# Kernel tuning notes

Hardware: AMD Instinct MI355X
Metric: run time of the kernel (lower is better)

## Reference

```python
import jax, jax.numpy as jnp
import numpy as np

N = 50000    # nodes
E = 640000   # edges (avg degree ~12.8)
D = 128      # feature dim (input = hidden = output)
L = 3        # num_layers
BN_EPS = 1e-5


def setup_inputs() -> dict:
    key = jax.random.key(0)
    ks = jax.random.split(key, 6)
    x = jax.random.normal(ks[0], (N, D), dtype=jnp.float32)
    edge_index = jax.random.randint(ks[1], (2, E), 0, N, dtype=jnp.int32)
    s = 1.0 / np.sqrt(D)
    # Weights stored as (in, out); equivalent to torch Linear's x @ W.T with W:(out,in).
    W1 = jax.random.normal(ks[2], (L, D, D), dtype=jnp.float32) * s
    b1 = jnp.zeros((L, D), dtype=jnp.float32)
    gamma = jnp.ones((L, D), dtype=jnp.float32)   # BatchNorm weight
    beta = jnp.zeros((L, D), dtype=jnp.float32)   # BatchNorm bias
    W2 = jax.random.normal(ks[3], (L, D, D), dtype=jnp.float32) * s
    b2 = jnp.zeros((L, D), dtype=jnp.float32)
    return {"x": x, "W1": W1, "b1": b1, "gamma": gamma, "beta": beta,
            "W2": W2, "b2": b2, "edge_index": edge_index}


def reference(x, W1, b1, gamma, beta, W2, b2, edge_index):
    src = edge_index[0]
    dst = edge_index[1]
    h = x
    for i in range(L):
        # GINConv aggregation: sum of source-node features into destinations, eps=0
        agg = jax.ops.segment_sum(h[src], dst, num_segments=N)   # [N, D]
        z = h + agg                                              # (1+eps)*x + sum_j x_j
        # MLP: Linear -> BatchNorm1d (training stats) -> ReLU -> Linear
        z = z @ W1[i] + b1[i]
        mu = jnp.mean(z, axis=0)
        var = jnp.mean((z - mu) ** 2, axis=0)                    # biased var (torch BN)
        z = (z - mu) * jax.lax.rsqrt(var + BN_EPS) * gamma[i] + beta[i]
        z = jax.nn.relu(z)
        z = z @ W2[i] + b2[i]
        # inter-layer ReLU (dropout_rate=0 -> identity)
        h = jax.nn.relu(z) if i < L - 1 else z
    return h
```

## Files before the change

kernel.cpp:

```cpp
#include <hip/hip_runtime.h>

#define D 128
#define BN_EPS 1e-5f
#define ELLW 64

typedef __bf16 bf16_t;
typedef __bf16 bf16x8 __attribute__((ext_vector_type(8)));
typedef __bf16 bf16x4 __attribute__((ext_vector_type(4)));
typedef __bf16 bf16x2 __attribute__((ext_vector_type(2)));
typedef float floatx4 __attribute__((ext_vector_type(4)));

__global__ void prep(const float* __restrict__ x, bf16_t* __restrict__ hb,
                     const float* __restrict__ W1, const float* __restrict__ W2,
                     bf16_t* __restrict__ Wsw, int* __restrict__ deg,
                     float* __restrict__ stats, int N, int n4) {
  int i = blockIdx.x * blockDim.x + threadIdx.x;
  if (i < n4) {
    float4 v = ((const float4*)x)[i];
    bf16x4 p;
    p[0] = (bf16_t)v.x; p[1] = (bf16_t)v.y; p[2] = (bf16_t)v.z; p[3] = (bf16_t)v.w;
    *(bf16x4*)(hb + (size_t)4 * i) = p;
  }
  if (i < N) deg[i] = 0;
  if (i < 768) stats[i] = 0.f;
  if (i < 6 * 16384) {
    int mat = i >> 14;
    int kn = i & 16383;
    int k = kn >> 7;
    int n = kn & 127;
    const float* Wm = (mat < 3) ? (W1 + (size_t)mat * 16384)
                                : (W2 + (size_t)(mat - 3) * 16384);
    float v = Wm[kn];
    int f = ((n >> 4) << 2) | (k >> 5);
    int ln = (((k >> 3) & 3) << 4) | (n & 15);
    int j = k & 7;
    Wsw[(size_t)mat * 16384 + ((f << 6) + ln) * 8 + j] = (bf16_t)v;
  }
}

__global__ void ell_fill(const int* __restrict__ src, const int* __restrict__ dst,
                         int* __restrict__ deg, int* __restrict__ ell, int E) {
  int e = blockIdx.x * blockDim.x + threadIdx.x;
  if (e < E) {
    int d = dst[e];
    int slot = atomicAdd(&deg[d], 1);
    if (slot < ELLW) ell[(size_t)d * ELLW + slot] = src[e];
  }
}

__global__ __launch_bounds__(256) void aggregate(
    const bf16_t* __restrict__ h, bf16_t* __restrict__ z,
    const int* __restrict__ ell, const int* __restrict__ deg, int Nn) {
  int node = blockIdx.x * 4 + (threadIdx.x >> 6);
  if (node >= Nn) return;
  int lane = threadIdx.x & 63;
  int off = lane << 1;
  int dg = deg[node]; if (dg > ELLW) dg = ELLW;
  const int* nb = ell + (size_t)node * ELLW;

  bf16x2 sv = *(const bf16x2*)(h + (size_t)node * D + off);
  float a0x = (float)sv[0], a0y = (float)sv[1];
  float a1x = 0.f, a1y = 0.f, a2x = 0.f, a2y = 0.f, a3x = 0.f, a3y = 0.f;
  int e = 0;
  for (; e + 4 <= dg; e += 4) {
    int4 i4 = *(const int4*)(nb + e);
    bf16x2 v0 = *(const bf16x2*)(h + (size_t)i4.x * D + off);
    bf16x2 v1 = *(const bf16x2*)(h + (size_t)i4.y * D + off);
    bf16x2 v2 = *(const bf16x2*)(h + (size_t)i4.z * D + off);
    bf16x2 v3 = *(const bf16x2*)(h + (size_t)i4.w * D + off);
    a0x += (float)v0[0]; a0y += (float)v0[1];
    a1x += (float)v1[0]; a1y += (float)v1[1];
    a2x += (float)v2[0]; a2y += (float)v2[1];
    a3x += (float)v3[0]; a3y += (float)v3[1];
  }
  for (; e < dg; ++e) {
    bf16x2 v = *(const bf16x2*)(h + (size_t)nb[e] * D + off);
    a0x += (float)v[0]; a0y += (float)v[1];
  }
  a0x += a1x + a2x + a3x;
  a0y += a1y + a2y + a3y;
  bf16x2 o;
  o[0] = (bf16_t)a0x; o[1] = (bf16_t)a0y;
  *(bf16x2*)(z + (size_t)node * D + off) = o;
}

__global__ __launch_bounds__(256) void gemm1_stats(
    const bf16_t* __restrict__ Z, const bf16_t* __restrict__ Wsw,
    const float* __restrict__ bias, bf16_t* __restrict__ Yf,
    float* __restrict__ stats, int nStrips, int N) {
  __shared__ bf16_t T[64][136];
  __shared__ float sred[256];
  const int t = threadIdx.x;
  const int wv = t >> 6;
  const int lane = t & 63;
  const int l15 = lane & 15;
  const int quad = lane >> 4;
  const int strip = blockIdx.x * 4 + wv;
  const bool active = strip < nStrips;

  sred[t] = 0.f;

  bf16x8 a[4];
  const int row = strip * 16 + l15;
  if (active && row < N) {
#pragma unroll
    for (int kc = 0; kc < 4; ++kc)
      a[kc] = *(const bf16x8*)(Z + (size_t)row * D + kc * 32 + quad * 8);
  } else {
#pragma unroll
    for (int kc = 0; kc < 4; ++kc)
#pragma unroll
      for (int j = 0; j < 8; ++j) a[kc][j] = (bf16_t)0.f;
  }

  floatx4 acc[8];
#pragma unroll
  for (int nt = 0; nt < 8; ++nt) {
    float bv = bias[nt * 16 + l15];
    acc[nt] = (floatx4){bv, bv, bv, bv};
  }

#pragma unroll
  for (int nt = 0; nt < 8; ++nt) {
#pragma unroll
    for (int kc = 0; kc < 4; ++kc) {
      bf16x8 b = *(const bf16x8*)(Wsw + (size_t)((nt * 4 + kc) * 64 + lane) * 8);
      acc[nt] = __builtin_amdgcn_mfma_f32_16x16x32_bf16(a[kc], b, acc[nt], 0, 0, 0);
    }
  }

  const int lr = wv * 16 + quad * 4;
#pragma unroll
  for (int nt = 0; nt < 8; ++nt) {
    int c = nt * 16 + l15;
#pragma unroll
    for (int r = 0; r < 4; ++r) T[lr + r][c] = (bf16_t)acc[nt][r];
  }
  __syncthreads();
  if (active) {
#pragma unroll
    for (int kc = 0; kc < 4; ++kc) {
      bf16x8 yv = *(const bf16x8*)&T[wv * 16 + l15][kc * 32 + quad * 8];
      *(bf16x8*)(Yf + ((size_t)(strip * 4 + kc) * 64 + lane) * 8) = yv;
    }
  }

  const int rowBase = strip * 16 + quad * 4;
#pragma unroll
  for (int nt = 0; nt < 8; ++nt) {
    int c = nt * 16 + l15;
    float s = 0.f, q = 0.f;
    if (active) {
#pragma unroll
      for (int r = 0; r < 4; ++r) {
        if (rowBase + r < N) {
          float v = acc[nt][r];
          s += v; q += v * v;
        }
      }
    }
    s += __shfl_xor(s, 16); s += __shfl_xor(s, 32);
    q += __shfl_xor(q, 16); q += __shfl_xor(q, 32);
    if (quad == 0) {
      atomicAdd(&sred[c], s);
      atomicAdd(&sred[128 + c], q);
    }
  }
  __syncthreads();
  atomicAdd(&stats[t], sred[t]);
}

__global__ __launch_bounds__(256) void mlp2(
    const bf16_t* __restrict__ Yf, const float* __restrict__ stats,
    const float* __restrict__ gamma, const float* __restrict__ beta,
    const bf16_t* __restrict__ Wsw, const float* __restrict__ bias,
    void* __restrict__ outp, int nStrips, int N, float invN,
    int relu_out, int fp32_out) {
  __shared__ float abL[256];
  const int t = threadIdx.x;
  if (t < 128) {
    float mu = stats[t] * invN;
    float var = fmaxf(stats[128 + t] * invN - mu * mu, 0.f);
    float a = gamma[t] * rsqrtf(var + BN_EPS);
    abL[t] = a;
    abL[128 + t] = beta[t] - mu * a;
  }
  __syncthreads();

  const int wv = t >> 6;
  const int lane = t & 63;
  const int l15 = lane & 15;
  const int quad = lane >> 4;
  const int strip = blockIdx.x * 4 + wv;
  if (strip >= nStrips) return;

  bf16x8 a2[4];
#pragma unroll
  for (int kc = 0; kc < 4; ++kc) {
    bf16x8 y = *(const bf16x8*)(Yf + ((size_t)(strip * 4 + kc) * 64 + lane) * 8);
#pragma unroll
    for (int j = 0; j < 8; ++j) {
      int c = kc * 32 + quad * 8 + j;
      float v = fmaxf(fmaf((float)y[j], abL[c], abL[128 + c]), 0.f);
      a2[kc][j] = (bf16_t)v;
    }
  }

  floatx4 acc[8];
#pragma unroll
  for (int nt = 0; nt < 8; ++nt) {
    float bv = bias[nt * 16 + l15];
    acc[nt] = (floatx4){bv, bv, bv, bv};
  }

#pragma unroll
  for (int nt = 0; nt < 8; ++nt) {
#pragma unroll
    for (int kc = 0; kc < 4; ++kc) {
      bf16x8 b = *(const bf16x8*)(Wsw + (size_t)((nt * 4 + kc) * 64 + lane) * 8);
      acc[nt] = __builtin_amdgcn_mfma_f32_16x16x32_bf16(a2[kc], b, acc[nt], 0, 0, 0);
    }
  }

  const int rowBase = strip * 16 + quad * 4;
  if (fp32_out) {
    float* out = (float*)outp;
#pragma unroll
    for (int nt = 0; nt < 8; ++nt) {
      int c = nt * 16 + l15;
#pragma unroll
      for (int r = 0; r < 4; ++r) {
        int row = rowBase + r;
        if (row < N) {
          float v = acc[nt][r];
          if (relu_out) v = fmaxf(v, 0.f);
          out[(size_t)row * D + c] = v;
        }
      }
    }
  } else {
    bf16_t* out = (bf16_t*)outp;
#pragma unroll
    for (int nt = 0; nt < 8; ++nt) {
      int c = nt * 16 + l15;
#pragma unroll
      for (int r = 0; r < 4; ++r) {
        int row = rowBase + r;
        if (row < N) {
          float v = acc[nt][r];
          if (relu_out) v = fmaxf(v, 0.f);
          out[(size_t)row * D + c] = (bf16_t)v;
        }
      }
    }
  }
}

extern "C" void kernel_launch(void* const* d_in, const int* in_sizes, int n_in,
                              void* d_out, int out_size, void* d_ws, size_t ws_size,
                              hipStream_t stream) {
  const float* x     = (const float*)d_in[0];
  const float* W1    = (const float*)d_in[1];
  const float* b1    = (const float*)d_in[2];
  const float* gamma = (const float*)d_in[3];
  const float* beta  = (const float*)d_in[4];
  const float* W2    = (const float*)d_in[5];
  const float* b2    = (const float*)d_in[6];
  const int*   ei    = (const int*)d_in[7];

  const int N = in_sizes[0] / D;
  const int E = in_sizes[7] / 2;
  const int* src = ei;
  const int* dst = ei + E;
  float* out = (float*)d_out;

  char* ws = (char*)d_ws;
  size_t bufBytes = (size_t)N * D * sizeof(bf16_t);
  bf16_t* hb   = (bf16_t*)ws;
  bf16_t* zb   = (bf16_t*)(ws + bufBytes);
  bf16_t* Yf   = (bf16_t*)(ws + 2 * bufBytes);
  int*    ell  = (int*)(ws + 3 * bufBytes);
  int*    deg  = (int*)((char*)ell + (size_t)N * ELLW * sizeof(int));
  float*  stats = (float*)((char*)deg + (size_t)N * sizeof(int));
  bf16_t* Wsw  = (bf16_t*)((char*)stats + 768 * sizeof(float));

  const int n4 = N * D / 4;
  const int prepBlocks = (n4 + 255) / 256;
  const int eb = (E + 255) / 256;
  const int aggBlocks = (N + 3) / 4;
  const int nStrips = (N + 15) / 16;
  const int gemmBlocks = (nStrips + 3) / 4;
  const float invN = 1.f / (float)N;

  prep<<<prepBlocks, 256, 0, stream>>>(x, hb, W1, W2, Wsw, deg, stats, N, n4);
  ell_fill<<<eb, 256, 0, stream>>>(src, dst, deg, ell, E);

  for (int i = 0; i < 3; ++i) {
    float* st = stats + (size_t)i * 256;
    aggregate<<<aggBlocks, 256, 0, stream>>>(hb, zb, ell, deg, N);
    gemm1_stats<<<gemmBlocks, 256, 0, stream>>>(
        zb, Wsw + (size_t)i * 16384, b1 + (size_t)i * D, Yf, st, nStrips, N);
    void* Ob = (i == 2) ? d_out : (void*)hb;
    mlp2<<<gemmBlocks, 256, 0, stream>>>(
        Yf, st, gamma + (size_t)i * D, beta + (size_t)i * D,
        Wsw + (size_t)(i + 3) * 16384, b2 + (size_t)i * D,
        Ob, nStrips, N, invN, (i < 2) ? 1 : 0, (i == 2) ? 1 : 0);
  }
}
```

Measured before the change: 342.9 us.

## Fuse both MLP GEMMs into one kernel with grid-wide barrier for BN stats

Merges gemm1_stats and mlp2 into a single kernel that keeps the first GEMM output in shared memory. An atomic-counter spin barrier waits for global BatchNorm statistics before applying normalization and the second GEMM. This removes the intermediate Yf buffer write/read and one kernel launch per layer. It relies on all 782 blocks being co-resident, otherwise it can deadlock, and it adds spin-wait cost.

```diff
diff --git a/kernel.cpp b/kernel.cpp
--- a/kernel.cpp
+++ b/kernel.cpp
@@ -13,7 +13,8 @@
 __global__ void prep(const float* __restrict__ x, bf16_t* __restrict__ hb,
                      const float* __restrict__ W1, const float* __restrict__ W2,
                      bf16_t* __restrict__ Wsw, int* __restrict__ deg,
-                     float* __restrict__ stats, int N, int n4) {
+                     float* __restrict__ stats, int* __restrict__ cnts,
+                     int N, int n4) {
   int i = blockIdx.x * blockDim.x + threadIdx.x;
   if (i < n4) {
     float4 v = ((const float4*)x)[i];
@@ -23,6 +24,7 @@
   }
   if (i < N) deg[i] = 0;
   if (i < 768) stats[i] = 0.f;
+  if (i < 3) cnts[i] = 0;
   if (i < 6 * 16384) {
     int mat = i >> 14;
     int kn = i & 16383;
@@ -84,12 +86,17 @@
   *(bf16x2*)(z + (size_t)node * D + off) = o;
 }
 
-__global__ __launch_bounds__(256) void gemm1_stats(
-    const bf16_t* __restrict__ Z, const bf16_t* __restrict__ Wsw,
-    const float* __restrict__ bias, bf16_t* __restrict__ Yf,
-    float* __restrict__ stats, int nStrips, int N) {
+__global__ __launch_bounds__(256) void fused_mlp(
+    const bf16_t* __restrict__ zb, const bf16_t* __restrict__ Ws1,
+    const bf16_t* __restrict__ Ws2, const float* __restrict__ b1l,
+    const float* __restrict__ b2l, const float* __restrict__ gl,
+    const float* __restrict__ btl, float* __restrict__ st,
+    int* __restrict__ ctr, void* __restrict__ outp,
+    int nStrips, int N, float invN, int relu_out, int fp32_out, int nBlocks) {
   __shared__ bf16_t T[64][136];
   __shared__ float sred[256];
+  __shared__ float abL[256];
+
   const int t = threadIdx.x;
   const int wv = t >> 6;
   const int lane = t & 63;
@@ -105,7 +112,7 @@
   if (active && row < N) {
 #pragma unroll
     for (int kc = 0; kc < 4; ++kc)
-      a[kc] = *(const bf16x8*)(Z + (size_t)row * D + kc * 32 + quad * 8);
+      a[kc] = *(const bf16x8*)(zb + (size_t)row * D + kc * 32 + quad * 8);
   } else {
 #pragma unroll
     for (int kc = 0; kc < 4; ++kc)
@@ -116,15 +123,14 @@
   floatx4 acc[8];
 #pragma unroll
   for (int nt = 0; nt < 8; ++nt) {
-    float bv = bias[nt * 16 + l15];
+    float bv = b1l[nt * 16 + l15];
     acc[nt] = (floatx4){bv, bv, bv, bv};
   }
-
 #pragma unroll
   for (int nt = 0; nt < 8; ++nt) {
 #pragma unroll
     for (int kc = 0; kc < 4; ++kc) {
-      bf16x8 b = *(const bf16x8*)(Wsw + (size_t)((nt * 4 + kc) * 64 + lane) * 8);
+      bf16x8 b = *(const bf16x8*)(Ws1 + (size_t)((nt * 4 + kc) * 64 + lane) * 8);
       acc[nt] = __builtin_amdgcn_mfma_f32_16x16x32_bf16(a[kc], b, acc[nt], 0, 0, 0);
     }
   }
@@ -136,16 +142,9 @@
 #pragma unroll
     for (int r = 0; r < 4; ++r) T[lr + r][c] = (bf16_t)acc[nt][r];
   }
-  __syncthreads();
-  if (active) {
-#pragma unroll
-    for (int kc = 0; kc < 4; ++kc) {
-      bf16x8 yv = *(const bf16x8*)&T[wv * 16 + l15][kc * 32 + quad * 8];
-      *(bf16x8*)(Yf + ((size_t)(strip * 4 + kc) * 64 + lane) * 8) = yv;
-    }
-  }
 
   const int rowBase = strip * 16 + quad * 4;
+  __syncthreads();
 #pragma unroll
   for (int nt = 0; nt < 8; ++nt) {
     int c = nt * 16 + l15;
@@ -167,89 +166,83 @@
     }
   }
   __syncthreads();
-  atomicAdd(&stats[t], sred[t]);
-}
-
-__global__ __launch_bounds__(256) void mlp2(
-    const bf16_t* __restrict__ Yf, const float* __restrict__ stats,
-    const float* __restrict__ gamma, const float* __restrict__ beta,
-    const bf16_t* __restrict__ Wsw, const float* __restrict__ bias,
-    void* __restrict__ outp, int nStrips, int N, float invN,
-    int relu_out, int fp32_out) {
-  __shared__ float abL[256];
-  const int t = threadIdx.x;
+  atomicAdd(&st[t], sred[t]);
+  __threadfence();
+  __syncthreads();
+  if (t == 0) {
+    __hip_atomic_fetch_add(ctr, 1, __ATOMIC_RELEASE, __HIP_MEMORY_SCOPE_AGENT);
+    while (__hip_atomic_load(ctr, __ATOMIC_ACQUIRE, __HIP_MEMORY_SCOPE_AGENT)
+           < nBlocks) { }
+  }
+  __syncthreads();
+
   if (t < 128) {
-    float mu = stats[t] * invN;
-    float var = fmaxf(stats[128 + t] * invN - mu * mu, 0.f);
-    float a = gamma[t] * rsqrtf(var + BN_EPS);
-    abL[t] = a;
-    abL[128 + t] = beta[t] - mu * a;
-  }
-  __syncthreads();
-
-  const int wv = t >> 6;
-  const int lane = t & 63;
-  const int l15 = lane & 15;
-  const int quad = lane >> 4;
-  const int strip = blockIdx.x * 4 + wv;
-  if (strip >= nStrips) return;
-
-  bf16x8 a2[4];
-#pragma unroll
-  for (int kc = 0; kc < 4; ++kc) {
-    bf16x8 y = *(const bf16x8*)(Yf + ((size_t)(strip * 4 + kc) * 64 + lane) * 8);
-#pragma unroll
-    for (int j = 0; j < 8; ++j) {
-      int c = kc * 32 + quad * 8 + j;
-      float v = fmaxf(fmaf((float)y[j], abL[c], abL[128 + c]), 0.f);
-      a2[kc][j] = (bf16_t)v;
-    }
-  }
-
-  floatx4 acc[8];
-#pragma unroll
-  for (int nt = 0; nt < 8; ++nt) {
-    float bv = bias[nt * 16 + l15];
-    acc[nt] = (floatx4){bv, bv, bv, bv};
-  }
-
-#pragma unroll
-  for (int nt = 0; nt < 8; ++nt) {
+    float s = __hip_atomic_load(&st[t], __ATOMIC_RELAXED, __HIP_MEMORY_SCOPE_AGENT);
+    float q = __hip_atomic_load(&st[128 + t], __ATOMIC_RELAXED, __HIP_MEMORY_SCOPE_AGENT);
+    float mu = s * invN;
+    float var = fmaxf(q * invN - mu * mu, 0.f);
+    float av = gl[t] * rsqrtf(var + BN_EPS);
+    abL[t] = av;
+    abL[128 + t] = btl[t] - mu * av;
+  }
+  __syncthreads();
+
+  if (active) {
+    bf16x8 a2[4];
 #pragma unroll
     for (int kc = 0; kc < 4; ++kc) {
-      bf16x8 b = *(const bf16x8*)(Wsw + (size_t)((nt * 4 + kc) * 64 + lane) * 8);
-      acc[nt] = __builtin_amdgcn_mfma_f32_16x16x32_bf16(a2[kc], b, acc[nt], 0, 0, 0);
-    }
-  }
-
-  const int rowBase = strip * 16 + quad * 4;
-  if (fp32_out) {
-    float* out = (float*)outp;
+      bf16x8 y = *(const bf16x8*)&T[wv * 16 + l15][kc * 32 + quad * 8];
+#pragma unroll
+      for (int j = 0; j < 8; ++j) {
+        int c = kc * 32 + quad * 8 + j;
+        float v = fmaxf(fmaf((float)y[j], abL[c], abL[128 + c]), 0.f);
+        a2[kc][j] = (bf16_t)v;
+      }
+    }
+
+    floatx4 acc2[8];
 #pragma unroll
     for (int nt = 0; nt < 8; ++nt) {
-      int c = nt * 16 + l15;
-#pragma unroll
-      for (int r = 0; r < 4; ++r) {
-        int row = rowBase + r;
-        if (row < N) {
-          float v = acc[nt][r];
-          if (relu_out) v = fmaxf(v, 0.f);
-          out[(size_t)row * D + c] = v;
+      float bv = b2l[nt * 16 + l15];
+      acc2[nt] = (floatx4){bv, bv, bv, bv};
+    }
+#pragma unroll
+    for (int nt = 0; nt < 8; ++nt) {
+#pragma unroll
+      for (int kc = 0; kc < 4; ++kc) {
+        bf16x8 b = *(const bf16x8*)(Ws2 + (size_t)((nt * 4 + kc) * 64 + lane) * 8);
+        acc2[nt] = __builtin_amdgcn_mfma_f32_16x16x32_bf16(a2[kc], b, acc2[nt], 0, 0, 0);
+      }
+    }
+
+    if (fp32_out) {
+      float* out = (float*)outp;
+#pragma unroll
+      for (int nt = 0; nt < 8; ++nt) {
+        int c = nt * 16 + l15;
+#pragma unroll
+        for (int r = 0; r < 4; ++r) {
+          int rw = rowBase + r;
+          if (rw < N) {
+            float v = acc2[nt][r];
+            if (relu_out) v = fmaxf(v, 0.f);
+            out[(size_t)rw * D + c] = v;
+          }
         }
       }
-    }
-  } else {
-    bf16_t* out = (bf16_t*)outp;
-#pragma unroll
-    for (int nt = 0; nt < 8; ++nt) {
-      int c = nt * 16 + l15;
-#pragma unroll
-      for (int r = 0; r < 4; ++r) {
-        int row = rowBase + r;
-        if (row < N) {
-          float v = acc[nt][r];
-          if (relu_out) v = fmaxf(v, 0.f);
-          out[(size_t)row * D + c] = (bf16_t)v;
+    } else {
+      bf16_t* out = (bf16_t*)outp;
+#pragma unroll
+      for (int nt = 0; nt < 8; ++nt) {
+        int c = nt * 16 + l15;
+#pragma unroll
+        for (int r = 0; r < 4; ++r) {
+          int rw = rowBase + r;
+          if (rw < N) {
+            float v = acc2[nt][r];
+            if (relu_out) v = fmaxf(v, 0.f);
+            out[(size_t)rw * D + c] = (bf16_t)v;
+          }
         }
       }
     }
@@ -278,11 +271,11 @@
   size_t bufBytes = (size_t)N * D * sizeof(bf16_t);
   bf16_t* hb   = (bf16_t*)ws;
   bf16_t* zb   = (bf16_t*)(ws + bufBytes);
-  bf16_t* Yf   = (bf16_t*)(ws + 2 * bufBytes);
-  int*    ell  = (int*)(ws + 3 * bufBytes);
+  int*    ell  = (int*)(ws + 2 * bufBytes);
   int*    deg  = (int*)((char*)ell + (size_t)N * ELLW * sizeof(int));
   float*  stats = (float*)((char*)deg + (size_t)N * sizeof(int));
-  bf16_t* Wsw  = (bf16_t*)((char*)stats + 768 * sizeof(float));
+  int*    cnts = (int*)((char*)stats + 768 * sizeof(float));
+  bf16_t* Wsw  = (bf16_t*)((char*)cnts + 16);
 
   const int n4 = N * D / 4;
   const int prepBlocks = (n4 + 255) / 256;
@@ -292,18 +285,18 @@
   const int gemmBlocks = (nStrips + 3) / 4;
   const float invN = 1.f / (float)N;
 
-  prep<<<prepBlocks, 256, 0, stream>>>(x, hb, W1, W2, Wsw, deg, stats, N, n4);
+  prep<<<prepBlocks, 256, 0, stream>>>(x, hb, W1, W2, Wsw, deg, stats, cnts, N, n4);
   ell_fill<<<eb, 256, 0, stream>>>(src, dst, deg, ell, E);
 
   for (int i = 0; i < 3; ++i) {
     float* st = stats + (size_t)i * 256;
     aggregate<<<aggBlocks, 256, 0, stream>>>(hb, zb, ell, deg, N);
-    gemm1_stats<<<gemmBlocks, 256, 0, stream>>>(
-        zb, Wsw + (size_t)i * 16384, b1 + (size_t)i * D, Yf, st, nStrips, N);
     void* Ob = (i == 2) ? d_out : (void*)hb;
-    mlp2<<<gemmBlocks, 256, 0, stream>>>(
-        Yf, st, gamma + (size_t)i * D, beta + (size_t)i * D,
-        Wsw + (size_t)(i + 3) * 16384, b2 + (size_t)i * D,
-        Ob, nStrips, N, invN, (i < 2) ? 1 : 0, (i == 2) ? 1 : 0);
-  }
-}
+    fused_mlp<<<gemmBlocks, 256, 0, stream>>>(
+        zb, Wsw + (size_t)i * 16384, Wsw + (size_t)(i + 3) * 16384,
+        b1 + (size_t)i * D, b2 + (size_t)i * D,
+        gamma + (size_t)i * D, beta + (size_t)i * D,
+        st, cnts + i, Ob, nStrips, N, invN,
+        (i < 2) ? 1 : 0, (i == 2) ? 1 : 0, gemmBlocks);
+  }
+}
```

Result: slower. 617.2 us (+80.0%).
